# Kernel tuning notes

Hardware: AMD Instinct MI355X
Metric: run time of the kernel (lower is better)

The kernel has to match this reference:

```python
import jax, jax.numpy as jnp
import numpy as np

K_HOPS = 2  # number_layers


def _gcn_norm(edge_index, edge_weight, num_nodes):
    # add self loops with weight 1 (PyG gcn_norm default, fill_value=1)
    row, col = edge_index[0], edge_index[1]
    loop = jnp.arange(num_nodes, dtype=edge_index.dtype)
    row = jnp.concatenate([row, loop])
    col = jnp.concatenate([col, loop])
    w = jnp.concatenate([edge_weight, jnp.ones((num_nodes,), edge_weight.dtype)])
    deg = jax.ops.segment_sum(w, col, num_segments=num_nodes)
    dinv = jnp.where(deg > 0, jax.lax.rsqrt(deg), 0.0)
    norm = dinv[row] * w * dinv[col]
    return row, col, norm


def setup_inputs() -> dict:
    key = jax.random.key(0)
    k1, k2, k3, k4 = jax.random.split(key, 4)
    N, E, F_IN, F_OUT = 100000, 1600000, 256, 40
    x = jax.random.normal(k1, (N, F_IN), dtype=jnp.float32)
    edge_index = jax.random.randint(k2, (2, E), 0, N, dtype=jnp.int64)
    edge_attr = jax.random.uniform(k3, (E,), dtype=jnp.float32)
    W = jax.random.normal(k4, (F_OUT, F_IN), dtype=jnp.float32) * (1.0 / np.sqrt(F_IN))
    b = jnp.zeros((F_OUT,), dtype=jnp.float32)
    return {"x": x, "edge_index": edge_index, "edge_attr": edge_attr, "W": W, "b": b}


def reference(x, edge_index, edge_attr, W, b):
    N = x.shape[0]
    row, col, norm = _gcn_norm(edge_index, edge_attr, N)
    for _ in range(K_HOPS):
        x = jax.ops.segment_sum(norm[:, None] * x[row], col, num_segments=N)
    out = x @ W.T + b           # SGConv final linear
    out = jax.nn.relu(out)      # dropout is a no-op in eval mode
    return jax.nn.log_softmax(out, axis=-1)
```

## Files before the change

kernel.cpp:

```cpp
#include <hip/hip_runtime.h>
#include <hip/hip_bf16.h>
#include <math.h>

#define TF_IN   256
#define TF_OUT  40
#define NCH2    5
#define BCAP    48
#define WQ      32767.0f


struct us8 { ushort4 a, b; };

__device__ inline float bf2f(unsigned short u) {
    union { unsigned int i; float f; } t; t.i = ((unsigned int)u) << 16; return t.f;
}
__device__ inline unsigned short f2bf(float f) {
    union { float f; unsigned int i; } t; t.f = f;
    unsigned int r = t.i + 0x7FFF + ((t.i >> 16) & 1);
    return (unsigned short)(r >> 16);
}

__device__ inline void acc8(float* acc, float v, const us8& h) {
    acc[0] += v * bf2f(h.a.x); acc[1] += v * bf2f(h.a.y);
    acc[2] += v * bf2f(h.a.z); acc[3] += v * bf2f(h.a.w);
    acc[4] += v * bf2f(h.b.x); acc[5] += v * bf2f(h.b.y);
    acc[6] += v * bf2f(h.b.z); acc[7] += v * bf2f(h.b.w);
}

__device__ inline void gather_acc(float* acc, const us8* __restrict__ hin,
                                  const unsigned int* __restrict__ b, int m,
                                  int chunk, const float* __restrict__ dinv) {
    int k = 0;
    for (; k + 4 <= m; k += 4) {
        uint4 e4 = *(const uint4*)(b + k);
        unsigned int r0 = e4.x >> 15, r1 = e4.y >> 15;
        unsigned int r2 = e4.z >> 15, r3 = e4.w >> 15;
        us8 h0 = hin[(size_t)r0 * NCH2 + chunk];
        us8 h1 = hin[(size_t)r1 * NCH2 + chunk];
        us8 h2 = hin[(size_t)r2 * NCH2 + chunk];
        us8 h3 = hin[(size_t)r3 * NCH2 + chunk];
        float v0 = dinv[r0] * ((float)(e4.x & 0x7FFF) * (1.0f / WQ));
        float v1 = dinv[r1] * ((float)(e4.y & 0x7FFF) * (1.0f / WQ));
        float v2 = dinv[r2] * ((float)(e4.z & 0x7FFF) * (1.0f / WQ));
        float v3 = dinv[r3] * ((float)(e4.w & 0x7FFF) * (1.0f / WQ));
        acc8(acc, v0, h0); acc8(acc, v1, h1);
        acc8(acc, v2, h2); acc8(acc, v3, h3);
    }
    for (; k < m; ++k) {
        unsigned int e = b[k];
        unsigned int r = e >> 15;
        us8 hv = hin[(size_t)r * NCH2 + chunk];
        float v = dinv[r] * ((float)(e & 0x7FFF) * (1.0f / WQ));
        acc8(acc, v, hv);
    }
}

__global__ void zero_kernel(int* __restrict__ cnt, int N) {
    int i = blockIdx.x * blockDim.x + threadIdx.x;
    if (i < N) cnt[i] = 0;
}

__global__ __launch_bounds__(256) void fused_gemm_scatter_kernel(
        const float* __restrict__ x, const float* __restrict__ W,
        unsigned short* __restrict__ h, int N, int gemmBlocks,
        const int* __restrict__ row, const int* __restrict__ col,
        const float* __restrict__ w, int* __restrict__ cnt,
        unsigned int* __restrict__ bucket, int E) {
    __shared__ float4 xs[128][8];
    __shared__ float4 wsm[40][9];
    int tid = threadIdx.x;

    if ((int)blockIdx.x < gemmBlocks) {
        int ng = tid >> 2;
        int jg = tid & 3;
        int j0 = jg * 10;
        int nodeBase = blockIdx.x * 128;
        int sk = (ng >> 1) & 7;

        float acc[2][10];
#pragma unroll
        for (int i = 0; i < 2; ++i)
#pragma unroll
            for (int j = 0; j < 10; ++j) acc[i][j] = 0.f;

        const float4* x4 = (const float4*)x;
        const float4* W4 = (const float4*)W;

        for (int kt = 0; kt < 8; ++kt) {
            int kb4 = kt * 8;
#pragma unroll
            for (int i = 0; i < 4; ++i) {
                int idx = tid + i * 256;
                int n = idx >> 3, c4 = idx & 7;
                int gn = nodeBase + n;
                float4 v = make_float4(0.f, 0.f, 0.f, 0.f);
                if (gn < N) v = x4[(size_t)gn * (TF_IN / 4) + kb4 + c4];
                xs[n][c4 ^ ((n >> 2) & 7)] = v;
            }
            {
                int idx = tid;
                int j = idx >> 3, c4 = idx & 7;
                wsm[j][c4] = W4[(size_t)j * (TF_IN / 4) + kb4 + c4];
                if (tid < 64) {
                    idx = tid + 256;
                    j = idx >> 3; c4 = idx & 7;
                    wsm[j][c4] = W4[(size_t)j * (TF_IN / 4) + kb4 + c4];
                }
            }
            __syncthreads();
#pragma unroll 2
            for (int c4 = 0; c4 < 8; ++c4) {
                int phys = c4 ^ sk;
                float4 xv0 = xs[ng * 2][phys];
                float4 xv1 = xs[ng * 2 + 1][phys];
#pragma unroll
                for (int jj = 0; jj < 10; ++jj) {
                    float4 wv = wsm[j0 + jj][c4];
                    acc[0][jj] += xv0.x * wv.x + xv0.y * wv.y + xv0.z * wv.z + xv0.w * wv.w;
                    acc[1][jj] += xv1.x * wv.x + xv1.y * wv.y + xv1.z * wv.z + xv1.w * wv.w;
                }
            }
            __syncthreads();
        }

#pragma unroll
        for (int i = 0; i < 2; ++i) {
            int gn = nodeBase + ng * 2 + i;
            if (gn < N) {
                ushort2* hp2 = (ushort2*)(h + (size_t)gn * TF_OUT + j0);
#pragma unroll
                for (int p = 0; p < 5; ++p) {
                    ushort2 o;
                    o.x = f2bf(acc[i][2 * p]);
                    o.y = f2bf(acc[i][2 * p + 1]);
                    hp2[p] = o;
                }
            }
        }
    } else {
        int base = ((int)blockIdx.x - gemmBlocks) * 1024 + tid * 4;
        if (base + 4 <= E) {
            int4   c4v = *(const int4*)(col + base);
            int4   r4v = *(const int4*)(row + base);
            float4 w4v = *(const float4*)(w + base);
            int p0 = atomicAdd(&cnt[c4v.x], 1);
            int p1 = atomicAdd(&cnt[c4v.y], 1);
            int p2 = atomicAdd(&cnt[c4v.z], 1);
            int p3 = atomicAdd(&cnt[c4v.w], 1);
            if (p0 < BCAP) bucket[(size_t)c4v.x * BCAP + p0] =
                ((unsigned int)r4v.x << 15) | (unsigned int)(w4v.x * WQ + 0.5f);
            if (p1 < BCAP) bucket[(size_t)c4v.y * BCAP + p1] =
                ((unsigned int)r4v.y << 15) | (unsigned int)(w4v.y * WQ + 0.5f);
            if (p2 < BCAP) bucket[(size_t)c4v.z * BCAP + p2] =
                ((unsigned int)r4v.z << 15) | (unsigned int)(w4v.z * WQ + 0.5f);
            if (p3 < BCAP) bucket[(size_t)c4v.w * BCAP + p3] =
                ((unsigned int)r4v.w << 15) | (unsigned int)(w4v.w * WQ + 0.5f);
        } else {
            for (int e = base; e < E; ++e) {
                int c = col[e];
                int pos = atomicAdd(&cnt[c], 1);
                if (pos < BCAP) {
                    unsigned int wq = (unsigned int)(w[e] * WQ + 0.5f);
                    bucket[(size_t)c * BCAP + pos] = ((unsigned int)row[e] << 15) | wq;
                }
            }
        }
    }
}

__global__ void deg_kernel(const unsigned int* __restrict__ bucket, const int* __restrict__ cnt,
                           float* __restrict__ dinv, int N) {
    int n = blockIdx.x * blockDim.x + threadIdx.x;
    if (n >= N) return;
    int m = cnt[n]; if (m > BCAP) m = BCAP;
    const unsigned int* b = bucket + (size_t)n * BCAP;
    float s = 1.0f;
    for (int k = 0; k < m; ++k) s += (float)(b[k] & 0x7FFF) * (1.0f / WQ);
    dinv[n] = rsqrtf(s);
}

__global__ __launch_bounds__(256) void hop_bf_kernel(
        const us8* __restrict__ hin, us8* __restrict__ hout,
        const int* __restrict__ cnt, const unsigned int* __restrict__ bucket,
        const float* __restrict__ dinv, int N) {
    int t = blockIdx.x * blockDim.x + threadIdx.x;
    int node  = t / NCH2;
    int chunk = t - node * NCH2;
    if (node >= N) return;

    float d = dinv[node];
    us8 a = hin[(size_t)node * NCH2 + chunk];
    float acc[8];
    acc[0] = bf2f(a.a.x) * d; acc[1] = bf2f(a.a.y) * d;
    acc[2] = bf2f(a.a.z) * d; acc[3] = bf2f(a.a.w) * d;
    acc[4] = bf2f(a.b.x) * d; acc[5] = bf2f(a.b.y) * d;
    acc[6] = bf2f(a.b.z) * d; acc[7] = bf2f(a.b.w) * d;

    int m = cnt[node]; if (m > BCAP) m = BCAP;
    gather_acc(acc, hin, bucket + (size_t)node * BCAP, m, chunk, dinv);

    us8 o;
    o.a.x = f2bf(acc[0] * d); o.a.y = f2bf(acc[1] * d);
    o.a.z = f2bf(acc[2] * d); o.a.w = f2bf(acc[3] * d);
    o.b.x = f2bf(acc[4] * d); o.b.y = f2bf(acc[5] * d);
    o.b.z = f2bf(acc[6] * d); o.b.w = f2bf(acc[7] * d);
    hout[(size_t)node * NCH2 + chunk] = o;
}

__global__ __launch_bounds__(320) void hop2_epi_kernel(
        const us8* __restrict__ hin, float4* __restrict__ out,
        const int* __restrict__ cnt, const unsigned int* __restrict__ bucket,
        const float* __restrict__ dinv, const float* __restrict__ bias, int N) {
    __shared__ float redm[320];
    __shared__ float reds[320];
    int tid = threadIdx.x;
    int g = tid / NCH2;
    int chunk = tid - g * NCH2;
    int node = blockIdx.x * 64 + g;
    bool valid = node < N;

    float acc[8];
#pragma unroll
    for (int j = 0; j < 8; ++j) acc[j] = 0.f;
    float d = 0.f;
    if (valid) {
        d = dinv[node];
        us8 a = hin[(size_t)node * NCH2 + chunk];
        acc[0] = bf2f(a.a.x) * d; acc[1] = bf2f(a.a.y) * d;
        acc[2] = bf2f(a.a.z) * d; acc[3] = bf2f(a.a.w) * d;
        acc[4] = bf2f(a.b.x) * d; acc[5] = bf2f(a.b.y) * d;
        acc[6] = bf2f(a.b.z) * d; acc[7] = bf2f(a.b.w) * d;
        int m = cnt[node]; if (m > BCAP) m = BCAP;
        gather_acc(acc, hin, bucket + (size_t)node * BCAP, m, chunk, dinv);
    }

    float v[8];
    float lm = -1e30f;
    if (valid) {
#pragma unroll
        for (int j = 0; j < 8; ++j) {
            float t2 = acc[j] * d + bias[chunk * 8 + j];
            t2 = fmaxf(t2, 0.f);
            v[j] = t2;
            lm = fmaxf(lm, t2);
        }
    }
    redm[tid] = lm;
    __syncthreads();
    float gm = redm[g * NCH2];
#pragma unroll
    for (int i = 1; i < NCH2; ++i) gm = fmaxf(gm, redm[g * NCH2 + i]);

    float ps = 0.f;
    if (valid) {
#pragma unroll
        for (int j = 0; j < 8; ++j) ps += __expf(v[j] - gm);
    }
    reds[tid] = ps;
    __syncthreads();
    float s = reds[g * NCH2];
#pragma unroll
    for (int i = 1; i < NCH2; ++i) s += reds[g * NCH2 + i];
    float lse = gm + __logf(s);

    if (valid) {
        float4 o0 = make_float4(v[0] - lse, v[1] - lse, v[2] - lse, v[3] - lse);
        float4 o1 = make_float4(v[4] - lse, v[5] - lse, v[6] - lse, v[7] - lse);
        out[(size_t)node * 10 + chunk * 2]     = o0;
        out[(size_t)node * 10 + chunk * 2 + 1] = o1;
    }
}

extern "C" void kernel_launch(void* const* d_in, const int* in_sizes, int n_in,
                              void* d_out, int out_size, void* d_ws, size_t ws_size,
                              hipStream_t stream) {
    const float* x  = (const float*)d_in[0];
    const int*   ei = (const int*)d_in[1];
    const float* ew = (const float*)d_in[2];
    const float* W  = (const float*)d_in[3];
    const float* b  = (const float*)d_in[4];

    const int F_out = in_sizes[4];
    const int F_in  = in_sizes[3] / F_out;
    const int N     = in_sizes[0] / F_in;
    const int E     = in_sizes[2];
    const int* row = ei;
    const int* col = ei + E;

    char* ws = (char*)d_ws;
    size_t off = 0;
    auto alloc = [&](size_t bytes) {
        void* p = ws + off;
        off += (bytes + 255) & ~(size_t)255;
        return p;
    };

    int*          cnt    = (int*)          alloc((size_t)N * 4);
    float*        dinv   = (float*)        alloc((size_t)N * 4);
    unsigned int* bucket = (unsigned int*) alloc((size_t)N * BCAP * 4);
    unsigned short* h0   = (unsigned short*)alloc((size_t)N * TF_OUT * 2);
    unsigned short* h1   = (unsigned short*)alloc((size_t)N * TF_OUT * 2);

    const int tb = 256;
    hipLaunchKernelGGL(zero_kernel, dim3((N + tb - 1) / tb), dim3(tb), 0, stream, cnt, N);

    int gemmBlocks    = (N + 127) / 128;
    int scatterBlocks = (E + 1023) / 1024;
    hipLaunchKernelGGL(fused_gemm_scatter_kernel, dim3(gemmBlocks + scatterBlocks), dim3(256),
                       0, stream, x, W, h0, N, gemmBlocks, row, col, ew, cnt, bucket, E);

    hipLaunchKernelGGL(deg_kernel, dim3((N + tb - 1) / tb), dim3(tb), 0, stream,
                       bucket, cnt, dinv, N);

    int hop1Threads = N * NCH2;
    hipLaunchKernelGGL(hop_bf_kernel, dim3((hop1Threads + tb - 1) / tb), dim3(tb), 0, stream,
                       (const us8*)h0, (us8*)h1, cnt, bucket, dinv, N);

    int hop2Blocks = (N + 63) / 64;
    hipLaunchKernelGGL(hop2_epi_kernel, dim3(hop2Blocks), dim3(320), 0, stream,
                       (const us8*)h1, (float4*)d_out, cnt, bucket, dinv, b, N);
}
```

Before: 331.3 us.

## Stage neighbor indices and weights in LDS; interleave GEMM and scatter blocks

Each hop kernel now has the five chunk threads of a node cooperatively load its bucket entries once, look up dinv for each source, and store row index and normalized weight in shared memory. Before, each of the five threads re-read the bucket and dinv on its own. The fused GEMM/scatter launch interleaves scatter blocks (now one edge per thread) with GEMM blocks so atomics and compute overlap across the grid. Degree summation now uses integer accumulation over vectorized loads. These add shared memory use and a block-wide barrier, and may lower occupancy.

```diff
diff --git a/kernel.cpp b/kernel.cpp
--- a/kernel.cpp
+++ b/kernel.cpp
@@ -27,34 +27,6 @@
     acc[6] += v * bf2f(h.b.z); acc[7] += v * bf2f(h.b.w);
 }
 
-__device__ inline void gather_acc(float* acc, const us8* __restrict__ hin,
-                                  const unsigned int* __restrict__ b, int m,
-                                  int chunk, const float* __restrict__ dinv) {
-    int k = 0;
-    for (; k + 4 <= m; k += 4) {
-        uint4 e4 = *(const uint4*)(b + k);
-        unsigned int r0 = e4.x >> 15, r1 = e4.y >> 15;
-        unsigned int r2 = e4.z >> 15, r3 = e4.w >> 15;
-        us8 h0 = hin[(size_t)r0 * NCH2 + chunk];
-        us8 h1 = hin[(size_t)r1 * NCH2 + chunk];
-        us8 h2 = hin[(size_t)r2 * NCH2 + chunk];
-        us8 h3 = hin[(size_t)r3 * NCH2 + chunk];
-        float v0 = dinv[r0] * ((float)(e4.x & 0x7FFF) * (1.0f / WQ));
-        float v1 = dinv[r1] * ((float)(e4.y & 0x7FFF) * (1.0f / WQ));
-        float v2 = dinv[r2] * ((float)(e4.z & 0x7FFF) * (1.0f / WQ));
-        float v3 = dinv[r3] * ((float)(e4.w & 0x7FFF) * (1.0f / WQ));
-        acc8(acc, v0, h0); acc8(acc, v1, h1);
-        acc8(acc, v2, h2); acc8(acc, v3, h3);
-    }
-    for (; k < m; ++k) {
-        unsigned int e = b[k];
-        unsigned int r = e >> 15;
-        us8 hv = hin[(size_t)r * NCH2 + chunk];
-        float v = dinv[r] * ((float)(e & 0x7FFF) * (1.0f / WQ));
-        acc8(acc, v, hv);
-    }
-}
-
 __global__ void zero_kernel(int* __restrict__ cnt, int N) {
     int i = blockIdx.x * blockDim.x + threadIdx.x;
     if (i < N) cnt[i] = 0;
@@ -62,19 +34,22 @@
 
 __global__ __launch_bounds__(256) void fused_gemm_scatter_kernel(
         const float* __restrict__ x, const float* __restrict__ W,
-        unsigned short* __restrict__ h, int N, int gemmBlocks,
+        unsigned short* __restrict__ h, int N, int gemmBlocks, int R,
         const int* __restrict__ row, const int* __restrict__ col,
         const float* __restrict__ w, int* __restrict__ cnt,
         unsigned int* __restrict__ bucket, int E) {
     __shared__ float4 xs[128][8];
     __shared__ float4 wsm[40][9];
     int tid = threadIdx.x;
-
-    if ((int)blockIdx.x < gemmBlocks) {
+    int b = blockIdx.x;
+    int q = b / (R + 1);
+    int r = b - q * (R + 1);
+
+    if (r == R) {
         int ng = tid >> 2;
         int jg = tid & 3;
         int j0 = jg * 10;
-        int nodeBase = blockIdx.x * 128;
+        int nodeBase = q * 128;
         int sk = (ng >> 1) & 7;
 
         float acc[2][10];
@@ -138,31 +113,14 @@
             }
         }
     } else {
-        int base = ((int)blockIdx.x - gemmBlocks) * 1024 + tid * 4;
-        if (base + 4 <= E) {
-            int4   c4v = *(const int4*)(col + base);
-            int4   r4v = *(const int4*)(row + base);
-            float4 w4v = *(const float4*)(w + base);
-            int p0 = atomicAdd(&cnt[c4v.x], 1);
-            int p1 = atomicAdd(&cnt[c4v.y], 1);
-            int p2 = atomicAdd(&cnt[c4v.z], 1);
-            int p3 = atomicAdd(&cnt[c4v.w], 1);
-            if (p0 < BCAP) bucket[(size_t)c4v.x * BCAP + p0] =
-                ((unsigned int)r4v.x << 15) | (unsigned int)(w4v.x * WQ + 0.5f);
-            if (p1 < BCAP) bucket[(size_t)c4v.y * BCAP + p1] =
-                ((unsigned int)r4v.y << 15) | (unsigned int)(w4v.y * WQ + 0.5f);
-            if (p2 < BCAP) bucket[(size_t)c4v.z * BCAP + p2] =
-                ((unsigned int)r4v.z << 15) | (unsigned int)(w4v.z * WQ + 0.5f);
-            if (p3 < BCAP) bucket[(size_t)c4v.w * BCAP + p3] =
-                ((unsigned int)r4v.w << 15) | (unsigned int)(w4v.w * WQ + 0.5f);
-        } else {
-            for (int e = base; e < E; ++e) {
-                int c = col[e];
-                int pos = atomicAdd(&cnt[c], 1);
-                if (pos < BCAP) {
-                    unsigned int wq = (unsigned int)(w[e] * WQ + 0.5f);
-                    bucket[(size_t)c * BCAP + pos] = ((unsigned int)row[e] << 15) | wq;
-                }
+        int sIdx = q * R + r;
+        int e = sIdx * 256 + tid;
+        if (e < E) {
+            int c = col[e];
+            int pos = atomicAdd(&cnt[c], 1);
+            if (pos < BCAP) {
+                unsigned int wq = (unsigned int)(w[e] * WQ + 0.5f);
+                bucket[(size_t)c * BCAP + pos] = ((unsigned int)row[e] << 15) | wq;
             }
         }
     }
@@ -174,21 +132,82 @@
     if (n >= N) return;
     int m = cnt[n]; if (m > BCAP) m = BCAP;
     const unsigned int* b = bucket + (size_t)n * BCAP;
-    float s = 1.0f;
-    for (int k = 0; k < m; ++k) s += (float)(b[k] & 0x7FFF) * (1.0f / WQ);
+    unsigned int si = 0;
+    int k = 0;
+    for (; k + 4 <= m; k += 4) {
+        uint4 e4 = *(const uint4*)(b + k);
+        si += (e4.x & 0x7FFF) + (e4.y & 0x7FFF) + (e4.z & 0x7FFF) + (e4.w & 0x7FFF);
+    }
+    for (; k < m; ++k) si += b[k] & 0x7FFF;
+    float s = 1.0f + (float)si * (1.0f / WQ);
     dinv[n] = rsqrtf(s);
 }
 
-__global__ __launch_bounds__(256) void hop_bf_kernel(
+__device__ inline void stage_rv(int g, int chunk, int m,
+                                const unsigned int* __restrict__ b,
+                                const float* __restrict__ dinv,
+                                int rs[64][BCAP + 1], float vs[64][BCAP + 1]) {
+    int k0 = chunk * 10;
+    unsigned int e[10];
+#pragma unroll
+    for (int i = 0; i < 10; ++i) {
+        int k = k0 + i;
+        e[i] = (k < m) ? b[k] : 0u;
+    }
+    float dv[10];
+#pragma unroll
+    for (int i = 0; i < 10; ++i) dv[i] = dinv[e[i] >> 15];
+#pragma unroll
+    for (int i = 0; i < 10; ++i) {
+        int k = k0 + i;
+        if (k < m) {
+            rs[g][k] = (int)(e[i] >> 15);
+            vs[g][k] = dv[i] * ((float)(e[i] & 0x7FFF) * (1.0f / WQ));
+        }
+    }
+}
+
+__device__ inline void gather_lds(float* acc, const us8* __restrict__ hin,
+                                  int g, int chunk, int m,
+                                  const int rs[64][BCAP + 1], const float vs[64][BCAP + 1]) {
+    int k = 0;
+    for (; k + 4 <= m; k += 4) {
+        int r0 = rs[g][k],     r1 = rs[g][k + 1];
+        int r2 = rs[g][k + 2], r3 = rs[g][k + 3];
+        us8 h0 = hin[(size_t)r0 * NCH2 + chunk];
+        us8 h1 = hin[(size_t)r1 * NCH2 + chunk];
+        us8 h2 = hin[(size_t)r2 * NCH2 + chunk];
+        us8 h3 = hin[(size_t)r3 * NCH2 + chunk];
+        acc8(acc, vs[g][k],     h0); acc8(acc, vs[g][k + 1], h1);
+        acc8(acc, vs[g][k + 2], h2); acc8(acc, vs[g][k + 3], h3);
+    }
+    for (; k < m; ++k) {
+        us8 hv = hin[(size_t)rs[g][k] * NCH2 + chunk];
+        acc8(acc, vs[g][k], hv);
+    }
+}
+
+__global__ __launch_bounds__(320) void hop_bf_kernel(
         const us8* __restrict__ hin, us8* __restrict__ hout,
         const int* __restrict__ cnt, const unsigned int* __restrict__ bucket,
         const float* __restrict__ dinv, int N) {
-    int t = blockIdx.x * blockDim.x + threadIdx.x;
-    int node  = t / NCH2;
-    int chunk = t - node * NCH2;
+    __shared__ int   rs[64][BCAP + 1];
+    __shared__ float vs[64][BCAP + 1];
+    int tid = threadIdx.x;
+    int g = tid / NCH2;
+    int chunk = tid - g * NCH2;
+    int node = blockIdx.x * 64 + g;
+
+    int m = 0;
+    float d = 0.f;
+    if (node < N) {
+        m = cnt[node]; if (m > BCAP) m = BCAP;
+        d = dinv[node];
+        stage_rv(g, chunk, m, bucket + (size_t)node * BCAP, dinv, rs, vs);
+    }
+    __syncthreads();
     if (node >= N) return;
 
-    float d = dinv[node];
     us8 a = hin[(size_t)node * NCH2 + chunk];
     float acc[8];
     acc[0] = bf2f(a.a.x) * d; acc[1] = bf2f(a.a.y) * d;
@@ -196,8 +215,7 @@
     acc[4] = bf2f(a.b.x) * d; acc[5] = bf2f(a.b.y) * d;
     acc[6] = bf2f(a.b.z) * d; acc[7] = bf2f(a.b.w) * d;
 
-    int m = cnt[node]; if (m > BCAP) m = BCAP;
-    gather_acc(acc, hin, bucket + (size_t)node * BCAP, m, chunk, dinv);
+    gather_lds(acc, hin, g, chunk, m, rs, vs);
 
     us8 o;
     o.a.x = f2bf(acc[0] * d); o.a.y = f2bf(acc[1] * d);
@@ -211,6 +229,8 @@
         const us8* __restrict__ hin, float4* __restrict__ out,
         const int* __restrict__ cnt, const unsigned int* __restrict__ bucket,
         const float* __restrict__ dinv, const float* __restrict__ bias, int N) {
+    __shared__ int   rs[64][BCAP + 1];
+    __shared__ float vs[64][BCAP + 1];
     __shared__ float redm[320];
     __shared__ float reds[320];
     int tid = threadIdx.x;
@@ -219,19 +239,25 @@
     int node = blockIdx.x * 64 + g;
     bool valid = node < N;
 
+    int m = 0;
+    float d = 0.f;
+    if (valid) {
+        m = cnt[node]; if (m > BCAP) m = BCAP;
+        d = dinv[node];
+        stage_rv(g, chunk, m, bucket + (size_t)node * BCAP, dinv, rs, vs);
+    }
+    __syncthreads();
+
     float acc[8];
 #pragma unroll
     for (int j = 0; j < 8; ++j) acc[j] = 0.f;
-    float d = 0.f;
-    if (valid) {
-        d = dinv[node];
+    if (valid) {
         us8 a = hin[(size_t)node * NCH2 + chunk];
         acc[0] = bf2f(a.a.x) * d; acc[1] = bf2f(a.a.y) * d;
         acc[2] = bf2f(a.a.z) * d; acc[3] = bf2f(a.a.w) * d;
         acc[4] = bf2f(a.b.x) * d; acc[5] = bf2f(a.b.y) * d;
         acc[6] = bf2f(a.b.z) * d; acc[7] = bf2f(a.b.w) * d;
-        int m = cnt[node]; if (m > BCAP) m = BCAP;
-        gather_acc(acc, hin, bucket + (size_t)node * BCAP, m, chunk, dinv);
+        gather_lds(acc, hin, g, chunk, m, rs, vs);
     }
 
     float v[8];
@@ -305,18 +331,18 @@
     hipLaunchKernelGGL(zero_kernel, dim3((N + tb - 1) / tb), dim3(tb), 0, stream, cnt, N);
 
     int gemmBlocks    = (N + 127) / 128;
-    int scatterBlocks = (E + 1023) / 1024;
-    hipLaunchKernelGGL(fused_gemm_scatter_kernel, dim3(gemmBlocks + scatterBlocks), dim3(256),
-                       0, stream, x, W, h0, N, gemmBlocks, row, col, ew, cnt, bucket, E);
+    int scatterBlocks = (E + 255) / 256;
+    int R             = (scatterBlocks + gemmBlocks - 1) / gemmBlocks;
+    hipLaunchKernelGGL(fused_gemm_scatter_kernel, dim3((R + 1) * gemmBlocks), dim3(256),
+                       0, stream, x, W, h0, N, gemmBlocks, R, row, col, ew, cnt, bucket, E);
 
     hipLaunchKernelGGL(deg_kernel, dim3((N + tb - 1) / tb), dim3(tb), 0, stream,
                        bucket, cnt, dinv, N);
 
-    int hop1Threads = N * NCH2;
-    hipLaunchKernelGGL(hop_bf_kernel, dim3((hop1Threads + tb - 1) / tb), dim3(tb), 0, stream,
+    int hopBlocks = (N + 63) / 64;
+    hipLaunchKernelGGL(hop_bf_kernel, dim3(hopBlocks), dim3(320), 0, stream,
                        (const us8*)h0, (us8*)h1, cnt, bucket, dinv, N);
 
-    int hop2Blocks = (N + 63) / 64;
-    hipLaunchKernelGGL(hop2_epi_kernel, dim3(hop2Blocks), dim3(320), 0, stream,
+    hipLaunchKernelGGL(hop2_epi_kernel, dim3(hopBlocks), dim3(320), 0, stream,
                        (const us8*)h1, (float4*)d_out, cnt, bucket, dinv, b, N);
 }
```

Result: slower. 346.0 us (+4.4%).
